# Kernel tuning notes

Hardware: AMD Instinct MI355X
Metric: run time of the kernel (lower is better)

The kernel has to match this reference:

```python
import jax, jax.numpy as jnp
import numpy as np

NUM_HEADS = 16

def setup_inputs() -> dict:
    key = jax.random.key(0)
    ks = jax.random.split(key, 3)
    B, S, D = 2, 2048, 1024
    x = jax.random.normal(ks[0], (B, S, D), dtype=jnp.float32)
    # xavier-uniform style scaling for weights
    Wqkv = jax.random.normal(ks[1], (3 * D, D), dtype=jnp.float32) * (1.0 / jnp.sqrt(D))
    bqkv = jnp.zeros((3 * D,), dtype=jnp.float32)
    Wo = jax.random.normal(ks[2], (D, D), dtype=jnp.float32) * (1.0 / jnp.sqrt(D))
    bo = jnp.zeros((D,), dtype=jnp.float32)
    return {"x": x, "Wqkv": Wqkv, "bqkv": bqkv, "Wo": Wo, "bo": bo}

def reference(x, Wqkv, bqkv, Wo, bo):
    B, S, D = x.shape
    H = NUM_HEADS
    hd = D // H
    # qkv projection (torch Linear: x @ W.T + b)
    qkv = x @ Wqkv.T + bqkv                      # [B, S, 3D]
    qkv = qkv.reshape(B, S, H, 3 * hd).transpose(0, 2, 1, 3)  # [B, H, S, 3hd]
    q, k, v = jnp.split(qkv, 3, axis=-1)         # each [B, H, S, hd]
    scale = 1.0 / jnp.sqrt(jnp.asarray(hd, dtype=x.dtype))
    logits = jnp.einsum('bhqd,bhkd->bhqk', q, k) * scale  # [B, H, S, S]
    attn = jax.nn.softmax(logits, axis=-1)
    vals = jnp.einsum('bhqk,bhkd->bhqd', attn, v)         # [B, H, S, hd]
    vals = vals.transpose(0, 2, 1, 3).reshape(B, S, D)
    return vals @ Wo.T + bo
```

## Files before the change

kernel.cpp:

```cpp
#include <hip/hip_runtime.h>


typedef short short8 __attribute__((ext_vector_type(8)));
typedef unsigned short ushort8v __attribute__((ext_vector_type(8)));
typedef unsigned short ushort4v __attribute__((ext_vector_type(4)));
typedef float floatx4 __attribute__((ext_vector_type(4)));

#define S_LEN 2048
#define D_MODEL 1024
#define N_HEADS 16
#define HEAD_DIM 64

#define EXP2F(x) __builtin_amdgcn_exp2f(x)

__device__ inline float bf2f(unsigned int u16) {
    union { unsigned int i; float f; } v; v.i = u16 << 16; return v.f;
}
__device__ inline unsigned short f2b(float f) {
    union { float f; unsigned int u; } v; v.f = f;
    return (unsigned short)((v.u + 0x7FFFu + ((v.u >> 16) & 1u)) >> 16);
}
__device__ inline unsigned int fbits(float f) {
    union { float f; unsigned int u; } v; v.f = f; return v.u;
}
__device__ inline unsigned int pack_bf2(float lo, float hi) {
    return __byte_perm(fbits(lo) + 0x8000u, fbits(hi) + 0x8000u, 0x7632);
}

__device__ inline int key128(int c) {
    return (c & 0x63) | ((c & 0x0C) << 1) | ((c & 0x10) >> 2);
}

__device__ inline void gld_lds16(const unsigned short* g, unsigned short* lds) {
    __builtin_amdgcn_global_load_lds(
        (const __attribute__((address_space(1))) void*)g,
        (__attribute__((address_space(3))) void*)lds, 16, 0, 0);
}

__global__ __launch_bounds__(256)
void cvt3(const float* __restrict__ s0, const float* __restrict__ s1,
          const float* __restrict__ s2,
          unsigned short* __restrict__ d0, unsigned short* __restrict__ d1,
          unsigned short* __restrict__ d2,
          int n0, int n1, int n2) {
    const int total = n0 + n1 + n2;
    for (int g = blockIdx.x * blockDim.x + threadIdx.x; g < total;
         g += gridDim.x * blockDim.x) {
        const float* s; unsigned short* d; int l;
        if (g < n0)            { s = s0; d = d0; l = g; }
        else if (g < n0 + n1)  { s = s1; d = d1; l = g - n0; }
        else                   { s = s2; d = d2; l = g - n0 - n1; }
        const float4* sp = (const float4*)s + (size_t)l * 2;
        float4 f0 = sp[0], f1 = sp[1];
        ushort8v o;
        o[0] = f2b(f0.x); o[1] = f2b(f0.y); o[2] = f2b(f0.z); o[3] = f2b(f0.w);
        o[4] = f2b(f1.x); o[5] = f2b(f1.y); o[6] = f2b(f1.z); o[7] = f2b(f1.w);
        *(ushort8v*)(d + (size_t)l * 8) = o;
    }
}

__device__ inline void stage_u(const unsigned short* __restrict__ g, int ldk,
                               unsigned short* lds, int wave, int lane) {
    const int lr  = lane >> 3;
    const int csw = ((lane & 7) ^ lr) * 8;
    gld_lds16(g + (size_t)(wave * 8 + lr) * ldk + csw, lds + wave * 512);
}

#define STAGE_A(kk0, buf) do {                                                 \
    _Pragma("unroll")                                                          \
    for (int u = 0; u < 4; ++u)                                                \
        stage_u(Abase + (size_t)(u * 64) * K + (kk0), K,                       \
                &AS[buf][u * 4096], wave, lane);                               \
} while (0)
#define STAGE_B2(kk0, buf) do {                                 \
    stage_u(Bbase + (kk0),                    K, &BS[buf][0],    wave, lane);  \
    stage_u(Bbase + (size_t)64 * K + (kk0),   K, &BS[buf][4096], wave, lane);  \
} while (0)
#define STAGE_B1(kk0, buf) do {                                    \
    stage_u(Bbase + (size_t)128 * K + (kk0),  K, &BS[buf][8192], wave, lane);  \
} while (0)

#define QLDB(pBx) do {                                                         \
    _Pragma("unroll")                                                          \
    for (int nj = 0; nj < 3; ++nj) {                                           \
        bF[nj][0] = *(const short8*)((pBx) + nj * 1024 + co0);                 \
        bF[nj][1] = *(const short8*)((pBx) + nj * 1024 + co1);                 \
    }                                                                          \
} while (0)

#define QPHASE(pAx, mq, ...) do {                                              \
    short8 aF[2][2];                                                           \
    _Pragma("unroll")                                                          \
    for (int m2 = 0; m2 < 2; ++m2) {                                           \
        aF[m2][0] = *(const short8*)((pAx) + ((mq) * 2 + m2) * 1024 + co0);    \
        aF[m2][1] = *(const short8*)((pAx) + ((mq) * 2 + m2) * 1024 + co1);    \
    }                                                                          \
    __VA_ARGS__;                                                               \
    __builtin_amdgcn_s_barrier();                                              \
    __builtin_amdgcn_s_setprio(1);                                             \
    _Pragma("unroll")                                                          \
    for (int kk = 0; kk < 2; ++kk)                                             \
        _Pragma("unroll")                                                      \
        for (int m2 = 0; m2 < 2; ++m2)                                         \
            _Pragma("unroll")                                                  \
            for (int nj = 0; nj < 3; ++nj)                                     \
                acc[(mq) * 2 + m2][nj] = __builtin_amdgcn_mfma_f32_16x16x32_bf16( \
                    aF[m2][kk], bF[nj][kk], acc[(mq) * 2 + m2][nj], 0, 0, 0);  \
    __builtin_amdgcn_s_setprio(0);                                             \
    __builtin_amdgcn_s_barrier();                                              \
} while (0)

#define WAIT_VM3() asm volatile("s_waitcnt vmcnt(3)" ::: "memory")
#define WAIT_VM0() asm volatile("s_waitcnt vmcnt(0)" ::: "memory")

__global__ __launch_bounds__(512, 2)
void qkv_gemm(const unsigned short* __restrict__ x,
              const unsigned short* __restrict__ Wqkv,
              const float* __restrict__ bqkv,
              unsigned short* __restrict__ Qb,
              unsigned short* __restrict__ Kb,
              unsigned short* __restrict__ Vb) {
    __shared__ unsigned short AS[2][16384];
    __shared__ unsigned short BS[2][12288];

    const int tid  = threadIdx.x;
    const int lane = tid & 63;
    const int wave = tid >> 6;
    const int wm = wave >> 2;
    const int wn = wave & 3;
    const int r  = lane & 15, q2 = lane >> 4;
    const int K  = D_MODEL;

    const int idx = blockIdx.x;
    const int swz = (idx & 7) * 32 + (idx >> 3);
    const int mb = swz & 15, nb = swz >> 4;
    const int m0 = mb * 256, n0 = nb * 192;

    const unsigned short* Abase = x    + (size_t)m0 * K;
    const unsigned short* Bbase = Wqkv + (size_t)n0 * K;

    const int co0 = ((q2 ^ (r & 7)) * 8);
    const int co1 = (((q2 + 4) ^ (r & 7)) * 8);
    const unsigned short* pA0 = &AS[0][(wm * 128 + r) * 64];
    const unsigned short* pA1 = &AS[1][(wm * 128 + r) * 64];
    const unsigned short* pB0 = &BS[0][(wn * 48 + r) * 64];
    const unsigned short* pB1 = &BS[1][(wn * 48 + r) * 64];

    floatx4 acc[8][3] = {};
    short8 bF[3][2];

    STAGE_A(0, 0);
    STAGE_B2(0, 0); STAGE_B1(0, 0);
    STAGE_B2(64, 1); STAGE_B1(64, 1);
    WAIT_VM3();
    __builtin_amdgcn_s_barrier();

    for (int i = 0; i < 8; ++i) {
        const bool more = (i < 7);
        const int kA1 = i * 128 + 64;
        const int kT2 = i * 128 + 128;
        const int kT3 = i * 128 + 192;

        QLDB(pB0);
        QPHASE(pA0, 0, { STAGE_A(kA1, 1); });
        QPHASE(pA0, 1, { if (more) STAGE_B2(kT2, 0); });
        QPHASE(pA0, 2, { if (more) STAGE_B1(kT2, 0); });
        QPHASE(pA0, 3, {
            if (more) { WAIT_VM3(); } else { WAIT_VM0(); }
        });
        QLDB(pB1);
        QPHASE(pA1, 0, { if (more) STAGE_A(kT2, 0); });
        QPHASE(pA1, 1, { if (more) STAGE_B2(kT3, 1); });
        QPHASE(pA1, 2, { if (more) STAGE_B1(kT3, 1); });
        QPHASE(pA1, 3, {
            if (more) { WAIT_VM3(); }
        });
    }

#pragma unroll
    for (int mi = 0; mi < 8; mi++) {
#pragma unroll
        for (int nj = 0; nj < 3; nj++) {
            int rem = wn * 48 + nj * 16 + r;
            int n = n0 + rem;
            int typ = rem >> 6;
            int d = rem & 63;
            float bv = bqkv[n];
            int m = m0 + wm * 128 + mi * 16 + q2 * 4;
            int b = m >> 11, s = m & 2047;
            if (typ == 2) {
                ushort4v pk;
#pragma unroll
                for (int rg = 0; rg < 4; rg++) pk[rg] = f2b(acc[mi][nj][rg] + bv);
                *(ushort4v*)(Vb + ((size_t)((b * N_HEADS + nb) * HEAD_DIM + d)) * S_LEN + s) = pk;
            } else {
                unsigned short* dst = (typ == 0) ? Qb : Kb;
                float sc = (typ == 0) ? 0.180336880f : 1.0f;
#pragma unroll
                for (int rg = 0; rg < 4; rg++)
                    dst[(((size_t)(b * N_HEADS + nb)) * S_LEN + s + rg) * HEAD_DIM + d] =
                        f2b((acc[mi][nj][rg] + bv) * sc);
            }
        }
    }
}

__global__ __launch_bounds__(256)
void out_gemm(const unsigned short* __restrict__ vals,
              const unsigned short* __restrict__ Wo,
              const float* __restrict__ bo,
              float* __restrict__ out) {
    __shared__ unsigned short As[2][8192];
    __shared__ unsigned short Bs[2][4096];

    const int tid  = threadIdx.x;
    const int lane = tid & 63;
    const int wave = tid >> 6;
    const int wm = wave >> 1, wn = wave & 1;
    const int r = lane & 15, q2 = lane >> 4;
    const int K = D_MODEL;
    const int m0 = blockIdx.y * 128;
    const int n0 = blockIdx.x * 64;

    const unsigned short* Abase = vals + (size_t)m0 * K;
    const unsigned short* Bbase = Wo   + (size_t)n0 * K;

    const int lr  = lane >> 3;
    const int csw = ((lane & 7) ^ lr) * 8;
    const int co0 = ((q2 ^ (r & 7)) * 8);
    const int co1 = (((q2 + 4) ^ (r & 7)) * 8);

    floatx4 acc[4][2] = {};

#define OSTAGE(k0, abuf, bbuf) do {                                            \
    _Pragma("unroll")                                                          \
    for (int u = 0; u < 4; ++u)                                                \
        gld_lds16(Abase + (size_t)(u * 32 + wave * 8 + lr) * K + (k0) + csw,   \
                  (abuf) + u * 2048 + wave * 512);                             \
    _Pragma("unroll")                                                          \
    for (int u = 0; u < 2; ++u)                                                \
        gld_lds16(Bbase + (size_t)(u * 32 + wave * 8 + lr) * K + (k0) + csw,   \
                  (bbuf) + u * 2048 + wave * 512);                             \
} while (0)

    OSTAGE(0, &As[0][0], &Bs[0][0]);
    __builtin_amdgcn_s_waitcnt(0);
    __syncthreads();

    int buf = 0;
    for (int k0 = 0; k0 < K; k0 += 64) {
        const bool more = (k0 + 64 < K);
        if (more) {
            OSTAGE(k0 + 64, &As[buf ^ 1][0], &Bs[buf ^ 1][0]);
        }
#pragma unroll
        for (int kk = 0; kk < 2; kk++) {
            const int co = kk ? co1 : co0;
            short8 aF[4], bF[2];
#pragma unroll
            for (int t = 0; t < 4; t++)
                aF[t] = *(const short8*)(&As[buf][(wm * 64 + t * 16 + r) * 64] + co);
#pragma unroll
            for (int t = 0; t < 2; t++)
                bF[t] = *(const short8*)(&Bs[buf][(wn * 32 + t * 16 + r) * 64] + co);
#pragma unroll
            for (int i = 0; i < 4; i++)
#pragma unroll
                for (int j = 0; j < 2; j++)
                    acc[i][j] = __builtin_amdgcn_mfma_f32_16x16x32_bf16(aF[i], bF[j], acc[i][j], 0, 0, 0);
        }
        if (more) {
            __builtin_amdgcn_s_waitcnt(0);
            __syncthreads();
            buf ^= 1;
        }
    }
#undef OSTAGE

#pragma unroll
    for (int i = 0; i < 4; i++) {
#pragma unroll
        for (int j = 0; j < 2; j++) {
            int n = n0 + wn * 32 + j * 16 + r;
            float bv = bo[n];
#pragma unroll
            for (int rg = 0; rg < 4; rg++) {
                int m = m0 + wm * 64 + i * 16 + q2 * 4 + rg;
                out[(size_t)m * D_MODEL + n] = acc[i][j][rg] + bv;
            }
        }
    }
}

__global__ __launch_bounds__(256, 2)
void attn_kernel(const unsigned short* __restrict__ Qb,
                 const unsigned short* __restrict__ Kb,
                 const unsigned short* __restrict__ Vg,
                 unsigned short* __restrict__ vals) {
    __shared__ unsigned short Ks[2 * 128 * 64];
    __shared__ unsigned short V3[3 * 128 * 64];

    const int tid = threadIdx.x;
    const int lane = tid & 63;
    const int wave = tid >> 6;
    const int r = lane & 15, q2 = lane >> 4;
    const int r7 = r & 7;
    const int w32 = wave * 32;

    const int idx  = blockIdx.x;
    const int xcd  = idx & 7;
    const int slot = idx >> 3;
    const int bh   = (xcd << 2) | (slot >> 4);
    const int q0   = (slot & 15) * 128;
    const int b = bh >> 4, h = bh & 15;

    const unsigned short* Qp = Qb + (size_t)bh * S_LEN * HEAD_DIM;
    const unsigned short* Kp = Kb + (size_t)bh * S_LEN * HEAD_DIM;
    const unsigned short* Vp = Vg + (size_t)bh * HEAD_DIM * S_LEN;

    const int srow = lane >> 3;
    const int scol = ((lane & 7) ^ srow) * 8;

    int krow[4], vd[4], vpan[4];
#pragma unroll
    for (int t = 0; t < 4; t++) {
        int c = wave * 32 + t * 8 + srow;
        krow[t] = key128(c);
        vpan[t] = c >> 6;
        vd[t]   = c & 63;
    }

    {
        const int qrow = tid >> 1;
        const int c0 = (tid & 1) * 4;
#pragma unroll
        for (int cc = 0; cc < 4; cc++) {
            int cb = c0 + cc;
            const uint4* gq = (const uint4*)(Qp + (size_t)(q0 + qrow) * HEAD_DIM + cb * 8);
            *(uint4*)(Ks + qrow * 64 + ((cb ^ (qrow & 7)) * 8)) = *gq;
        }
    }
    __syncthreads();
    short8 qf[2][2];
#pragma unroll
    for (int nt = 0; nt < 2; nt++)
#pragma unroll
        for (int ks = 0; ks < 2; ks++) {
            int cb = ks * 4 + q2;
            qf[nt][ks] = *(const short8*)(Ks + (w32 + nt * 16 + r) * 64 + ((cb ^ r7) * 8));
        }
    __syncthreads();

#pragma unroll
    for (int t = 0; t < 4; t++) {
        gld_lds16(Kp + (size_t)krow[t] * HEAD_DIM + scol,
                  Ks + (wave * 32 + t * 8) * 64);
        gld_lds16(Vp + (size_t)vd[t] * S_LEN + vpan[t] * 64 + scol,
                  V3 + (wave * 32 + t * 8) * 64);
    }
#pragma unroll
    for (int t = 0; t < 4; t++) {
        gld_lds16(Kp + (size_t)(128 + krow[t]) * HEAD_DIM + scol,
                  Ks + 8192 + (wave * 32 + t * 8) * 64);
        gld_lds16(Vp + (size_t)vd[t] * S_LEN + 128 + vpan[t] * 64 + scol,
                  V3 + 8192 + (wave * 32 + t * 8) * 64);
    }
    asm volatile("s_waitcnt vmcnt(8)" ::: "memory");
    __syncthreads();

    union { unsigned int u[4]; short8 s; } onesu;
    onesu.u[0] = 0x3F803F80u; onesu.u[1] = 0x3F803F80u;
    onesu.u[2] = 0x3F803F80u; onesu.u[3] = 0x3F803F80u;
    const short8 onesf = onesu.s;

    floatx4 l_acc[2] = {};
    floatx4 o_acc[2][4] = {};
    floatx4 sp[8][2];
    short8 paA[2][4];

#define AZERO() do {                                                           \
    _Pragma("unroll")                                                          \
    for (int mt = 0; mt < 8; mt++)                                             \
        _Pragma("unroll")                                                      \
        for (int nt = 0; nt < 2; nt++)                                         \
            sp[mt][nt] = (floatx4){0.f, 0.f, 0.f, 0.f};                        \
} while (0)

#define AQK(KBASE) do {                                                        \
    _Pragma("unroll")                                                          \
    for (int mt = 0; mt < 8; mt++)                                             \
        _Pragma("unroll")                                                      \
        for (int ks = 0; ks < 2; ks++) {                                       \
            int cb = ks * 4 + q2;                                              \
            short8 kfr = *(const short8*)(Ks + (KBASE) + (mt * 16 + r) * 64 + ((cb ^ r7) * 8)); \
            _Pragma("unroll")                                                  \
            for (int nt = 0; nt < 2; nt++)                                     \
                sp[mt][nt] = __builtin_amdgcn_mfma_f32_16x16x32_bf16(kfr, qf[nt][ks], sp[mt][nt], 0, 0, 0); \
        }                                                                      \
} while (0)

#define AEXPPACK() do {                                                        \
    _Pragma("unroll")                                                          \
    for (int nt = 0; nt < 2; nt++)                                             \
        _Pragma("unroll")                                                      \
        for (int mt = 0; mt < 8; mt++)                                         \
            _Pragma("unroll")                                                  \
            for (int reg = 0; reg < 4; reg++)                                  \
                sp[mt][nt][reg] = EXP2F(sp[mt][nt][reg]);                      \
    _Pragma("unroll")                                                          \
    for (int nt = 0; nt < 2; nt++)                                             \
        _Pragma("unroll")                                                      \
        for (int ks = 0; ks < 4; ks++) {                                       \
            union { unsigned int u[4]; short8 s; } tw;                         \
            tw.u[0] = pack_bf2(sp[2 * ks][nt][0],     sp[2 * ks][nt][1]);      \
            tw.u[1] = pack_bf2(sp[2 * ks][nt][2],     sp[2 * ks][nt][3]);      \
            tw.u[2] = pack_bf2(sp[2 * ks + 1][nt][0], sp[2 * ks + 1][nt][1]);  \
            tw.u[3] = pack_bf2(sp[2 * ks + 1][nt][2], sp[2 * ks + 1][nt][3]);  \
            paA[nt][ks] = tw.s;                                                \
        }                                                                      \
} while (0)

#define APVL(VBASE) do {                                                       \
    _Pragma("unroll")                                                          \
    for (int dt = 0; dt < 4; dt++) {                                           \
        short8 vf[4];                                                          \
        _Pragma("unroll")                                                      \
        for (int ks = 0; ks < 4; ks++) {                                       \
            int cb = (ks & 1) * 4 + q2;                                        \
            vf[ks] = *(const short8*)(V3 + (VBASE) + (ks >> 1) * 4096 + (dt * 16 + r) * 64 + ((cb ^ r7) * 8)); \
        }                                                                      \
        _Pragma("unroll")                                                      \
        for (int nt = 0; nt < 2; nt++)                                         \
            _Pragma("unroll")                                                  \
            for (int ks = 0; ks < 4; ks++)                                     \
                o_acc[nt][dt] = __builtin_amdgcn_mfma_f32_16x16x32_bf16(paA[nt][ks], vf[ks], o_acc[nt][dt], 0, 0, 0); \
    }                                                                          \
    _Pragma("unroll")                                                          \
    for (int nt = 0; nt < 2; nt++)                                             \
        _Pragma("unroll")                                                      \
        for (int ks = 0; ks < 4; ks++)                                         \
            l_acc[nt] = __builtin_amdgcn_mfma_f32_16x16x32_bf16(paA[nt][ks], onesf, l_acc[nt], 0, 0, 0); \
} while (0)

    AZERO();
    __builtin_amdgcn_s_setprio(1);
    AQK(0);
    __builtin_amdgcn_s_setprio(0);
    AEXPPACK();

    for (int t = 0; t < 15; ++t) {
        asm volatile("s_waitcnt vmcnt(0)" ::: "memory");
        __syncthreads();
        if (t < 14) {
            const int kb  = (t & 1) * 8192;
            const int vs  = ((t + 2) % 3) * 8192;
            const int kt2 = (t + 2) * 128;
#pragma unroll
            for (int tt = 0; tt < 4; tt++) {
                gld_lds16(Kp + (size_t)(kt2 + krow[tt]) * HEAD_DIM + scol,
                          Ks + kb + (wave * 32 + tt * 8) * 64);
                gld_lds16(Vp + (size_t)vd[tt] * S_LEN + kt2 + vpan[tt] * 64 + scol,
                          V3 + vs + (wave * 32 + tt * 8) * 64);
            }
        }
        const int kc = ((t + 1) & 1) * 8192;
        const int vb = (t % 3) * 8192;
        AZERO();
        __builtin_amdgcn_s_setprio(1);
        AQK(kc);
        APVL(vb);
        __builtin_amdgcn_s_setprio(0);
        AEXPPACK();
    }

    __builtin_amdgcn_s_setprio(1);
    APVL(0);
    __builtin_amdgcn_s_setprio(0);

#undef AZERO
#undef AQK
#undef AEXPPACK
#undef APVL

#pragma unroll
    for (int nt = 0; nt < 2; nt++) {
#pragma unroll
        for (int reg = 0; reg < 4; reg++) {
            float inv = 1.0f / l_acc[nt][reg];
            int srow2 = q0 + w32 + nt * 16 + q2 * 4 + reg;
            size_t base = ((size_t)b * S_LEN + srow2) * D_MODEL + h * HEAD_DIM + r;
#pragma unroll
            for (int dt = 0; dt < 4; dt++)
                vals[base + dt * 16] = f2b(o_acc[nt][dt][reg] * inv);
        }
    }
}

extern "C" void kernel_launch(void* const* d_in, const int* in_sizes, int n_in,
                              void* d_out, int out_size, void* d_ws, size_t ws_size,
                              hipStream_t stream) {
    const float* x    = (const float*)d_in[0];
    const float* Wqkv = (const float*)d_in[1];
    const float* bqkv = (const float*)d_in[2];
    const float* Wo   = (const float*)d_in[3];
    const float* bo   = (const float*)d_in[4];
    float* out = (float*)d_out;

    const size_t NX = 4194304, NW = 3145728, NO = 1048576;
    unsigned short* xb    = (unsigned short*)d_ws;
    unsigned short* Wqkvb = xb + NX;
    unsigned short* Wob   = Wqkvb + NW;
    unsigned short* Qb    = Wob + NO;
    unsigned short* Kb    = Qb + NX;
    unsigned short* Vb    = Kb + NX;
    unsigned short* vals  = xb;

    cvt3<<<4096, 256, 0, stream>>>(x, Wqkv, Wo, xb, Wqkvb, Wob,
                                   (int)(NX / 8), (int)(NW / 8), (int)(NO / 8));
    qkv_gemm<<<256, 512, 0, stream>>>(xb, Wqkvb, bqkv, Qb, Kb, Vb);
    attn_kernel<<<512, 256, 0, stream>>>(Qb, Kb, Vb, vals);
    out_gemm<<<dim3(16, 32), 256, 0, stream>>>(vals, Wob, bo, out);
}
```

Measured before the change: 172.9 us.

## Retile QKV GEMM to 128x192 blocks with 4 waves

Shrinks the QKV projection GEMM tile from 256x192 with 8 waves to 128x192 with 4 waves, doubling the grid to 512 blocks. Each wave now computes a 64x96 sub-tile (4x6 MFMA accumulators) instead of 128x48, and the staging macros and wait counts are adjusted to match. The aim is to fill more of the chip's compute units and cut LDS use per block for better occupancy. The cost is lower arithmetic intensity per block, so the shared weight tiles are re-read from global memory twice as often.

```diff
diff --git a/kernel.cpp b/kernel.cpp
--- a/kernel.cpp
+++ b/kernel.cpp
@@ -69,90 +69,89 @@
 #define STAGE_A(kk0, buf) do {                                                 \
     _Pragma("unroll")                                                          \
     for (int u = 0; u < 4; ++u)                                                \
-        stage_u(Abase + (size_t)(u * 64) * K + (kk0), K,                       \
-                &AS[buf][u * 4096], wave, lane);                               \
-} while (0)
-#define STAGE_B2(kk0, buf) do {                                 \
-    stage_u(Bbase + (kk0),                    K, &BS[buf][0],    wave, lane);  \
-    stage_u(Bbase + (size_t)64 * K + (kk0),   K, &BS[buf][4096], wave, lane);  \
-} while (0)
-#define STAGE_B1(kk0, buf) do {                                    \
-    stage_u(Bbase + (size_t)128 * K + (kk0),  K, &BS[buf][8192], wave, lane);  \
+        stage_u(Abase + (size_t)(u * 32) * K + (kk0), K,                       \
+                &AS[buf][u * 2048], wave, lane);                               \
+} while (0)
+#define STAGE_B3a(kk0, buf) do {                               \
+    _Pragma("unroll")                                                          \
+    for (int u = 0; u < 3; ++u)                                                \
+        stage_u(Bbase + (size_t)(u * 32) * K + (kk0), K,                       \
+                &BS[buf][u * 2048], wave, lane);                               \
+} while (0)
+#define STAGE_B3b(kk0, buf) do {                             \
+    _Pragma("unroll")                                                          \
+    for (int u = 3; u < 6; ++u)                                                \
+        stage_u(Bbase + (size_t)(u * 32) * K + (kk0), K,                       \
+                &BS[buf][u * 2048], wave, lane);                               \
 } while (0)
 
 #define QLDB(pBx) do {                                                         \
     _Pragma("unroll")                                                          \
-    for (int nj = 0; nj < 3; ++nj) {                                           \
+    for (int nj = 0; nj < 6; ++nj) {                                           \
         bF[nj][0] = *(const short8*)((pBx) + nj * 1024 + co0);                 \
         bF[nj][1] = *(const short8*)((pBx) + nj * 1024 + co1);                 \
     }                                                                          \
 } while (0)
 
 #define QPHASE(pAx, mq, ...) do {                                              \
-    short8 aF[2][2];                                                           \
-    _Pragma("unroll")                                                          \
-    for (int m2 = 0; m2 < 2; ++m2) {                                           \
-        aF[m2][0] = *(const short8*)((pAx) + ((mq) * 2 + m2) * 1024 + co0);    \
-        aF[m2][1] = *(const short8*)((pAx) + ((mq) * 2 + m2) * 1024 + co1);    \
-    }                                                                          \
+    short8 aF0 = *(const short8*)((pAx) + (mq) * 1024 + co0);                  \
+    short8 aF1 = *(const short8*)((pAx) + (mq) * 1024 + co1);                  \
     __VA_ARGS__;                                                               \
     __builtin_amdgcn_s_barrier();                                              \
     __builtin_amdgcn_s_setprio(1);                                             \
     _Pragma("unroll")                                                          \
     for (int kk = 0; kk < 2; ++kk)                                             \
         _Pragma("unroll")                                                      \
-        for (int m2 = 0; m2 < 2; ++m2)                                         \
-            _Pragma("unroll")                                                  \
-            for (int nj = 0; nj < 3; ++nj)                                     \
-                acc[(mq) * 2 + m2][nj] = __builtin_amdgcn_mfma_f32_16x16x32_bf16( \
-                    aF[m2][kk], bF[nj][kk], acc[(mq) * 2 + m2][nj], 0, 0, 0);  \
+        for (int nj = 0; nj < 6; ++nj)                                         \
+            acc[mq][nj] = __builtin_amdgcn_mfma_f32_16x16x32_bf16(             \
+                kk ? aF1 : aF0, bF[nj][kk], acc[mq][nj], 0, 0, 0);             \
     __builtin_amdgcn_s_setprio(0);                                             \
     __builtin_amdgcn_s_barrier();                                              \
 } while (0)
 
-#define WAIT_VM3() asm volatile("s_waitcnt vmcnt(3)" ::: "memory")
+#define WAIT_VM6() asm volatile("s_waitcnt vmcnt(6)" ::: "memory")
 #define WAIT_VM0() asm volatile("s_waitcnt vmcnt(0)" ::: "memory")
 
-__global__ __launch_bounds__(512, 2)
+__global__ __launch_bounds__(256, 2)
 void qkv_gemm(const unsigned short* __restrict__ x,
               const unsigned short* __restrict__ Wqkv,
               const float* __restrict__ bqkv,
               unsigned short* __restrict__ Qb,
               unsigned short* __restrict__ Kb,
               unsigned short* __restrict__ Vb) {
-    __shared__ unsigned short AS[2][16384];
+    __shared__ unsigned short AS[2][8192];
     __shared__ unsigned short BS[2][12288];
 
     const int tid  = threadIdx.x;
     const int lane = tid & 63;
     const int wave = tid >> 6;
-    const int wm = wave >> 2;
-    const int wn = wave & 3;
+    const int wm = wave >> 1;
+    const int wn = wave & 1;
     const int r  = lane & 15, q2 = lane >> 4;
     const int K  = D_MODEL;
 
     const int idx = blockIdx.x;
-    const int swz = (idx & 7) * 32 + (idx >> 3);
-    const int mb = swz & 15, nb = swz >> 4;
-    const int m0 = mb * 256, n0 = nb * 192;
+    const int swz = (idx & 7) * 64 + (idx >> 3);
+    const int mb = swz & 31, nb = swz >> 5;
+    const int m0 = mb * 128, n0 = nb * 192;
 
     const unsigned short* Abase = x    + (size_t)m0 * K;
     const unsigned short* Bbase = Wqkv + (size_t)n0 * K;
 
     const int co0 = ((q2 ^ (r & 7)) * 8);
     const int co1 = (((q2 + 4) ^ (r & 7)) * 8);
-    const unsigned short* pA0 = &AS[0][(wm * 128 + r) * 64];
-    const unsigned short* pA1 = &AS[1][(wm * 128 + r) * 64];
-    const unsigned short* pB0 = &BS[0][(wn * 48 + r) * 64];
-    const unsigned short* pB1 = &BS[1][(wn * 48 + r) * 64];
-
-    floatx4 acc[8][3] = {};
-    short8 bF[3][2];
+    const unsigned short* pA0 = &AS[0][(wm * 64 + r) * 64];
+    const unsigned short* pA1 = &AS[1][(wm * 64 + r) * 64];
+    const unsigned short* pB0 = &BS[0][(wn * 96 + r) * 64];
+    const unsigned short* pB1 = &BS[1][(wn * 96 + r) * 64];
+
+    floatx4 acc[4][6] = {};
+    short8 bF[6][2];
 
     STAGE_A(0, 0);
-    STAGE_B2(0, 0); STAGE_B1(0, 0);
-    STAGE_B2(64, 1); STAGE_B1(64, 1);
-    WAIT_VM3();
+    STAGE_B3a(0, 0); STAGE_B3b(0, 0);
+    STAGE_B3a(64, 1); STAGE_B3b(64, 1);
+    WAIT_VM6();
     __builtin_amdgcn_s_barrier();
 
     for (int i = 0; i < 8; ++i) {
@@ -163,30 +162,30 @@
 
         QLDB(pB0);
         QPHASE(pA0, 0, { STAGE_A(kA1, 1); });
-        QPHASE(pA0, 1, { if (more) STAGE_B2(kT2, 0); });
-        QPHASE(pA0, 2, { if (more) STAGE_B1(kT2, 0); });
+        QPHASE(pA0, 1, { if (more) STAGE_B3a(kT2, 0); });
+        QPHASE(pA0, 2, { if (more) STAGE_B3b(kT2, 0); });
         QPHASE(pA0, 3, {
-            if (more) { WAIT_VM3(); } else { WAIT_VM0(); }
+            if (more) { WAIT_VM6(); } else { WAIT_VM0(); }
         });
         QLDB(pB1);
         QPHASE(pA1, 0, { if (more) STAGE_A(kT2, 0); });
-        QPHASE(pA1, 1, { if (more) STAGE_B2(kT3, 1); });
-        QPHASE(pA1, 2, { if (more) STAGE_B1(kT3, 1); });
+        QPHASE(pA1, 1, { if (more) STAGE_B3a(kT3, 1); });
+        QPHASE(pA1, 2, { if (more) STAGE_B3b(kT3, 1); });
         QPHASE(pA1, 3, {
-            if (more) { WAIT_VM3(); }
+            if (more) { WAIT_VM6(); }
         });
     }
 
 #pragma unroll
-    for (int mi = 0; mi < 8; mi++) {
-#pragma unroll
-        for (int nj = 0; nj < 3; nj++) {
-            int rem = wn * 48 + nj * 16 + r;
+    for (int mi = 0; mi < 4; mi++) {
+#pragma unroll
+        for (int nj = 0; nj < 6; nj++) {
+            int rem = wn * 96 + nj * 16 + r;
             int n = n0 + rem;
             int typ = rem >> 6;
             int d = rem & 63;
             float bv = bqkv[n];
-            int m = m0 + wm * 128 + mi * 16 + q2 * 4;
+            int m = m0 + wm * 64 + mi * 16 + q2 * 4;
             int b = m >> 11, s = m & 2047;
             if (typ == 2) {
                 ushort4v pk;
@@ -517,7 +516,7 @@
 
     cvt3<<<4096, 256, 0, stream>>>(x, Wqkv, Wo, xb, Wqkvb, Wob,
                                    (int)(NX / 8), (int)(NW / 8), (int)(NO / 8));
-    qkv_gemm<<<256, 512, 0, stream>>>(xb, Wqkvb, bqkv, Qb, Kb, Vb);
+    qkv_gemm<<<512, 256, 0, stream>>>(xb, Wqkvb, bqkv, Qb, Kb, Vb);
     attn_kernel<<<512, 256, 0, stream>>>(Qb, Kb, Vb, vals);
     out_gemm<<<dim3(16, 32), 256, 0, stream>>>(vals, Wob, bo, out);
 }
```

Result: no change. 171.5 us (-0.8%).
